# Kernel optimization log

Hardware: AMD Instinct MI355X
Metric: run time of the kernel (lower is better)

The kernel has to match this reference:

```python
import jax, jax.numpy as jnp
import numpy as np
import math

HEAD_DEPTH = 16
CLIP = 10.0
NEG_INF = 1.0e10
# combined scale: (1/sqrt(head_depth)) * log_50(400)
SCALE = (math.log(400.0) / math.log(50.0)) / math.sqrt(HEAD_DEPTH)


def setup_inputs() -> dict:
    key = jax.random.key(0)
    kq, kk, kv, km = jax.random.split(key, 4)
    B, H, S, D = 4, 8, 2048, HEAD_DEPTH
    Q = jax.random.normal(kq, (B, H, S, D), dtype=jnp.float32)
    K = jax.random.normal(kk, (B, H, S, D), dtype=jnp.float32)
    V = jax.random.normal(kv, (B, H, S, D), dtype=jnp.float32)
    # mask: (B, n_nodes, 1) bool; True -> masked (logit set to -inf)
    mask = jax.random.randint(km, (B, S, 1), 0, 2) == 1
    return {"Q": Q, "K": K, "V": V, "mask": mask}


def reference(Q, K, V, mask):
    # logits: (B, H, q_seq, k_seq)
    logits = jnp.einsum("bhqd,bhkd->bhqk", Q, K) * SCALE
    logits = CLIP * jnp.tanh(logits)  # tanh clip
    # mask[:, None, None, :, 0] -> (B, 1, 1, k_seq), True gets -inf
    m = mask[:, None, None, :, 0]
    logits = jnp.where(m, -NEG_INF, logits)
    probs = jax.nn.softmax(logits, axis=-1)
    return jnp.einsum("bhqk,bhkd->bhqd", probs, V)
```

## Files before the change

kernel.cpp:

```cpp
#include <hip/hip_runtime.h>


typedef __fp16 h2 __attribute__((ext_vector_type(2)));
typedef __fp16 h4 __attribute__((ext_vector_type(4)));
typedef float  f4 __attribute__((ext_vector_type(4)));

#define SEQ 2048
#define NBH 32
#define TPB 128
#define KWS_BYTES ((size_t)NBH * TPB * 64 * 8)
#define VWS_BYTES KWS_BYTES
#define BIAS_BYTES ((size_t)4 * SEQ * 4)
#define IDX_BYTES  ((size_t)4 * SEQ * 4)
#define META_BYTES 64
#define WS_NEEDED (KWS_BYTES + VWS_BYTES + BIAS_BYTES + IDX_BYTES + META_BYTES)

__device__ __forceinline__ float fast_exp2(float x) {
#if __has_builtin(__builtin_amdgcn_exp2f)
    return __builtin_amdgcn_exp2f(x);
#else
    return exp2f(x);
#endif
}

__device__ __forceinline__ float dot2acc(h2 a, float accv) {
#if __has_builtin(__builtin_amdgcn_fdot2)
    const h2 one = {(__fp16)1.0f, (__fp16)1.0f};
    return __builtin_amdgcn_fdot2(a, one, accv, false);
#else
    return accv + (float)a[0] + (float)a[1];
#endif
}

__global__ __launch_bounds__(256) void attn_scan(
    const int* __restrict__ maskp, int* __restrict__ idxws,
    float* __restrict__ biasws, int* __restrict__ meta)
{
    __shared__ int partial[256];
    const int b   = blockIdx.x;
    const int tid = threadIdx.x;

    int keep[8], cnt = 0;
    #pragma unroll
    for (int j = 0; j < 8; ++j) {
        keep[j] = (maskp[b * SEQ + tid * 8 + j] == 0);
        cnt += keep[j];
    }
    partial[tid] = cnt;
    __syncthreads();
    for (int off = 1; off < 256; off <<= 1) {
        int add = (tid >= off) ? partial[tid - off] : 0;
        __syncthreads();
        partial[tid] += add;
        __syncthreads();
    }
    const int total = partial[255];
    int pos = partial[tid] - cnt;
    #pragma unroll
    for (int j = 0; j < 8; ++j) {
        if (keep[j]) idxws[b * SEQ + pos++] = tid * 8 + j;
    }
    for (int i = tid; i < SEQ; i += 256) {
        biasws[b * SEQ + i] = (i < total) ? 0.0f : -1.0e30f;
        if (i >= total) idxws[b * SEQ + i] = 0;
    }
    if (tid == 0) {
        int nr = (total + 255) >> 8;
        meta[b] = nr < 1 ? 1 : nr;
    }
}

__global__ __launch_bounds__(256) void attn_prep(
    const float* __restrict__ Kp, const float* __restrict__ Vp,
    const int* __restrict__ idxws,
    __fp16* __restrict__ Kws, __fp16* __restrict__ Vws)
{
    const int tid = threadIdx.x;
    const int T   = blockIdx.x * 4 + (tid >> 6);
    const int l   = tid & 63;
    const int bh  = T >> 7;
    const int t   = T & (TPB - 1);
    const int b   = bh >> 3;
    const int c   = l & 15;
    const int g   = l >> 4;
    const size_t base = (size_t)bh * (SEQ * 16);
    const int*   idx  = idxws + (size_t)b * SEQ;

    {
        const int krow = idx[t * 16 + c];
        f4 kv = *(const f4*)(Kp + base + (size_t)krow * 16 + 4 * g);
        h2 k0 = __builtin_amdgcn_cvt_pkrtz(kv[0], kv[1]);
        h2 k1 = __builtin_amdgcn_cvt_pkrtz(kv[2], kv[3]);
        h4 kh; kh[0] = k0[0]; kh[1] = k0[1]; kh[2] = k1[0]; kh[3] = k1[1];
        *(h4*)(Kws + ((size_t)T * 64 + l) * 4) = kh;
    }
    {
        const int v0 = idx[t * 16 + 4 * g + 0];
        const int v1 = idx[t * 16 + 4 * g + 1];
        const int v2 = idx[t * 16 + 4 * g + 2];
        const int v3 = idx[t * 16 + 4 * g + 3];
        h2 p0 = __builtin_amdgcn_cvt_pkrtz(Vp[base + (size_t)v0 * 16 + c],
                                           Vp[base + (size_t)v1 * 16 + c]);
        h2 p1 = __builtin_amdgcn_cvt_pkrtz(Vp[base + (size_t)v2 * 16 + c],
                                           Vp[base + (size_t)v3 * 16 + c]);
        h4 vh; vh[0] = p0[0]; vh[1] = p0[1]; vh[2] = p1[0]; vh[3] = p1[1];
        *(h4*)(Vws + ((size_t)T * 64 + l) * 4) = vh;
    }
}

__global__ __launch_bounds__(512, 8) void attn_v5(
    const float* __restrict__ Qp, const __fp16* __restrict__ Kws,
    const __fp16* __restrict__ Vws, const float* __restrict__ biasws,
    const int* __restrict__ meta, float* __restrict__ out)
{
    __shared__ __align__(16) _Float16 Kbuf[2][4096];
    __shared__ __align__(16) _Float16 Vbuf[2][4096];
    __shared__ __align__(16) float    Bbuf[2][256];

    const int bid  = blockIdx.x;
    const int bh   = bid >> 5;
    const int qblk = bid & 31;
    const int b    = bh >> 3;
    const int tid  = threadIdx.x;
    const int wave = tid >> 6;
    const int lane = tid & 63;
    const int qt   = wave & 3;
    const int kg   = wave >> 2;
    const int c    = lane & 15;
    const int g    = lane >> 4;

    const size_t base  = (size_t)bh * (SEQ * 16);
    const int    qbase = qblk * 64 + qt * 16;
    const float  c1 = 1.1047809f;
    const float  c2 = -28.8539008f;

    const int nr = meta[b];

    h4 qfrag;
    {
        f4 qv = *(const f4*)(Qp + base + (size_t)(qbase + c) * 16 + 4 * g);
        h2 lo = __builtin_amdgcn_cvt_pkrtz(c1 * qv[0], c1 * qv[1]);
        h2 hi = __builtin_amdgcn_cvt_pkrtz(c1 * qv[2], c1 * qv[3]);
        qfrag[0] = lo[0]; qfrag[1] = lo[1]; qfrag[2] = hi[0]; qfrag[3] = hi[1];
    }

    const f4* ksrc = (const f4*)(Kws + (size_t)bh * TPB * 256);
    const f4* vsrc = (const f4*)(Vws + (size_t)bh * TPB * 256);
    const float* bsrc = biasws + (size_t)b * SEQ;

    f4 kpre = ksrc[tid];
    f4 vpre = vsrc[tid];
    float bpre = (tid < 256) ? bsrc[tid] : 0.0f;
    *(f4*)&Kbuf[0][tid * 8] = kpre;
    *(f4*)&Vbuf[0][tid * 8] = vpre;
    if (tid < 256) Bbuf[0][tid] = bpre;
    {
        const int r1 = (1 < nr) ? 1 : (nr - 1);
        kpre = ksrc[r1 * 512 + tid];
        vpre = vsrc[r1 * 512 + tid];
        if (tid < 256) bpre = bsrc[r1 * 256 + tid];
    }
    __syncthreads();

    f4 acc = {0.f, 0.f, 0.f, 0.f};
    float dsum = 0.f;

    for (int r = 0; r < nr; ++r) {
        const int cb = r & 1, nb = cb ^ 1;
        if (r + 1 < nr) {
            *(f4*)&Kbuf[nb][tid * 8] = kpre;
            *(f4*)&Vbuf[nb][tid * 8] = vpre;
            if (tid < 256) Bbuf[nb][tid] = bpre;
        }
        if (r + 2 < nr) {
            kpre = ksrc[(r + 2) * 512 + tid];
            vpre = vsrc[(r + 2) * 512 + tid];
            if (tid < 256) bpre = bsrc[(r + 2) * 256 + tid];
        }

        const _Float16* Kc = &Kbuf[cb][kg * 2048];
        const _Float16* Vc = &Vbuf[cb][kg * 2048];
        const float*    Bc = &Bbuf[cb][kg * 128];

        #pragma unroll
        for (int t = 0; t < 8; ++t) {
            h4 afrag = *(const h4*)(Kc + t * 256 + lane * 4);
            f4 s = __builtin_amdgcn_mfma_f32_16x16x16f16(
                afrag, qfrag, (f4){0.f, 0.f, 0.f, 0.f}, 0, 0, 0);

            f4 b4 = *(const f4*)(Bc + t * 16 + 4 * g);
            float p[4];
            #pragma unroll
            for (int i = 0; i < 4; ++i) {
                float tt = fast_exp2(s[i]);
                float w  = __builtin_amdgcn_rcpf(1.0f + tt);
                p[i] = fast_exp2(__builtin_fmaf(c2, w, b4[i]));
            }
            h2 plo = __builtin_amdgcn_cvt_pkrtz(p[0], p[1]);
            h2 phi = __builtin_amdgcn_cvt_pkrtz(p[2], p[3]);
            dsum = dot2acc(plo, dsum);
            dsum = dot2acc(phi, dsum);
            h4 pf; pf[0] = plo[0]; pf[1] = plo[1]; pf[2] = phi[0]; pf[3] = phi[1];

            h4 vfrag = *(const h4*)(Vc + t * 256 + lane * 4);
            acc = __builtin_amdgcn_mfma_f32_16x16x16f16(pf, vfrag, acc, 0, 0, 0);
        }
        __syncthreads();
    }

    dsum += __shfl_xor(dsum, 16);
    dsum += __shfl_xor(dsum, 32);

    float* ex = (float*)&Kbuf[0][0];
    const int slot = (qt * 64 + lane) * 5;
    if (kg == 1) {
        ex[slot + 0] = acc[0]; ex[slot + 1] = acc[1];
        ex[slot + 2] = acc[2]; ex[slot + 3] = acc[3];
        ex[slot + 4] = dsum;
    }
    __syncthreads();
    if (kg == 0) {
        const float dT = dsum + ex[slot + 4];
        #pragma unroll
        for (int i = 0; i < 4; ++i) {
            const float denom = __shfl(dT, 4 * g + i);
            out[base + (size_t)(qbase + 4 * g + i) * 16 + c] =
                (acc[i] + ex[slot + i]) / denom;
        }
    }
}

#define KROW 20
#define VROW 520

__global__ __launch_bounds__(512, 8) void attn_fwd_v3(
    const float* __restrict__ Qp, const float* __restrict__ Kp,
    const float* __restrict__ Vp, const int* __restrict__ maskp,
    float* __restrict__ out)
{
    __shared__ __align__(16) _Float16 Klds[512 * KROW];
    __shared__ __align__(16) _Float16 Vt[16 * VROW];
    __shared__ __align__(16) float biasf[512];

    const int bid  = blockIdx.x;
    const int bh   = bid >> 5;
    const int qblk = bid & 31;
    const int b    = bh >> 3;
    const int tid  = threadIdx.x;
    const int wave = tid >> 6;
    const int lane = tid & 63;
    const int qt   = wave & 3;
    const int kg   = wave >> 2;
    const int c    = lane & 15;
    const int g    = lane >> 4;

    const size_t base = (size_t)bh * (SEQ * 16);
    const int qbase = qblk * 64 + qt * 16;
    const float c1 = 1.1047809f;
    const float c2 = -28.8539008f;

    h4 qfrag;
    {
        f4 qv = *(const f4*)(Qp + base + (size_t)(qbase + c) * 16 + 4 * g);
        h2 lo = __builtin_amdgcn_cvt_pkrtz(c1 * qv[0], c1 * qv[1]);
        h2 hi = __builtin_amdgcn_cvt_pkrtz(c1 * qv[2], c1 * qv[3]);
        qfrag[0] = lo[0]; qfrag[1] = lo[1]; qfrag[2] = hi[0]; qfrag[3] = hi[1];
    }

    f4 acc = {0.f, 0.f, 0.f, 0.f};
    float dsum = 0.f;
    const int kgb = kg * 256;

    for (int round = 0; round < 4; ++round) {
        {
            const float* Kc = Kp + base + (size_t)round * (512 * 16);
            const float* Vc = Vp + base + (size_t)round * (512 * 16);
            #pragma unroll
            for (int j = 0; j < 4; ++j) {
                const int i = j * 512 + tid;
                f4 kv = *(const f4*)(Kc + (size_t)i * 4);
                f4 vv = *(const f4*)(Vc + (size_t)i * 4);
                const int key = i >> 2;
                const int dq  = (i & 3) * 4;
                h2 k0 = __builtin_amdgcn_cvt_pkrtz(kv[0], kv[1]);
                h2 k1 = __builtin_amdgcn_cvt_pkrtz(kv[2], kv[3]);
                h4 kh; kh[0] = k0[0]; kh[1] = k0[1]; kh[2] = k1[0]; kh[3] = k1[1];
                *(h4*)&Klds[key * KROW + dq] = kh;
                #pragma unroll
                for (int e = 0; e < 4; ++e)
                    Vt[(dq + e) * VROW + key] = (_Float16)vv[e];
            }
            biasf[tid] = maskp[(size_t)b * SEQ + round * 512 + tid] ? -60.0f : 0.0f;
        }
        __syncthreads();

        #pragma unroll
        for (int t = 0; t < 16; ++t) {
            const int kb = kgb + t * 16;
            h4 afrag = *(const h4*)&Klds[(kb + c) * KROW + 4 * g];
            f4 s = __builtin_amdgcn_mfma_f32_16x16x16f16(
                afrag, qfrag, (f4){0.f, 0.f, 0.f, 0.f}, 0, 0, 0);
            f4 b4 = *(const f4*)&biasf[kb + 4 * g];
            float p[4];
            #pragma unroll
            for (int i = 0; i < 4; ++i) {
                float tt = fast_exp2(s[i]);
                float w  = __builtin_amdgcn_rcpf(1.0f + tt);
                p[i] = fast_exp2(__builtin_fmaf(c2, w, b4[i]));
            }
            h2 plo = __builtin_amdgcn_cvt_pkrtz(p[0], p[1]);
            h2 phi = __builtin_amdgcn_cvt_pkrtz(p[2], p[3]);
            dsum = dot2acc(plo, dsum);
            dsum = dot2acc(phi, dsum);
            h4 pf; pf[0] = plo[0]; pf[1] = plo[1]; pf[2] = phi[0]; pf[3] = phi[1];
            h4 vfrag = *(const h4*)&Vt[c * VROW + kb + 4 * g];
            acc = __builtin_amdgcn_mfma_f32_16x16x16f16(pf, vfrag, acc, 0, 0, 0);
        }
        __syncthreads();
    }

    dsum += __shfl_xor(dsum, 16);
    dsum += __shfl_xor(dsum, 32);

    float* ex = (float*)Klds;
    const int slot = (qt * 64 + lane) * 5;
    if (kg == 1) {
        ex[slot + 0] = acc[0]; ex[slot + 1] = acc[1];
        ex[slot + 2] = acc[2]; ex[slot + 3] = acc[3];
        ex[slot + 4] = dsum;
    }
    __syncthreads();
    if (kg == 0) {
        const float dT = dsum + ex[slot + 4];
        #pragma unroll
        for (int i = 0; i < 4; ++i) {
            const float denom = __shfl(dT, 4 * g + i);
            out[base + (size_t)(qbase + 4 * g + i) * 16 + c] =
                (acc[i] + ex[slot + i]) / denom;
        }
    }
}

extern "C" void kernel_launch(void* const* d_in, const int* in_sizes, int n_in,
                              void* d_out, int out_size, void* d_ws, size_t ws_size,
                              hipStream_t stream) {
    const float* Q    = (const float*)d_in[0];
    const float* K    = (const float*)d_in[1];
    const float* V    = (const float*)d_in[2];
    const int*   mask = (const int*)d_in[3];
    float* out = (float*)d_out;

    if (ws_size >= WS_NEEDED) {
        char* p = (char*)d_ws;
        __fp16* Kws = (__fp16*)p;                       p += KWS_BYTES;
        __fp16* Vws = (__fp16*)p;                       p += VWS_BYTES;
        float*  Bws = (float*)p;                        p += BIAS_BYTES;
        int*    Iws = (int*)p;                          p += IDX_BYTES;
        int*    Mws = (int*)p;
        attn_scan<<<dim3(4), dim3(256), 0, stream>>>(mask, Iws, Bws, Mws);
        attn_prep<<<dim3(1024), dim3(256), 0, stream>>>(K, V, Iws, Kws, Vws);
        attn_v5<<<dim3(1024), dim3(512), 0, stream>>>(Q, Kws, Vws, Bws, Mws, out);
    } else {
        attn_fwd_v3<<<dim3(1024), dim3(512), 0, stream>>>(Q, K, V, mask, out);
    }
}
```

Measured before the change: 93.38 us.

## Load K/V fragments directly from global into registers, drop LDS staging

The attention kernel no longer stages K, V and bias tiles through double-buffered shared memory with per-round barriers. Each wave now reads its MFMA fragments straight from the pre-packed global workspace into a two-slot register prefetch ring, loading two tiles ahead. This removes the LDS writes and reads and the __syncthreads inside the loop. In exchange, the four query-tile waves that share a key group each fetch the same K/V data from global memory separately, so the kernel leans on L1/L2 hits and has less latency hiding.

```diff
diff --git a/kernel.cpp b/kernel.cpp
--- a/kernel.cpp
+++ b/kernel.cpp
@@ -108,14 +108,12 @@
     }
 }
 
-__global__ __launch_bounds__(512, 8) void attn_v5(
+__global__ __launch_bounds__(512, 8) void attn_v6(
     const float* __restrict__ Qp, const __fp16* __restrict__ Kws,
     const __fp16* __restrict__ Vws, const float* __restrict__ biasws,
     const int* __restrict__ meta, float* __restrict__ out)
 {
-    __shared__ __align__(16) _Float16 Kbuf[2][4096];
-    __shared__ __align__(16) _Float16 Vbuf[2][4096];
-    __shared__ __align__(16) float    Bbuf[2][256];
+    __shared__ float ex[1280];
 
     const int bid  = blockIdx.x;
     const int bh   = bid >> 5;
@@ -144,57 +142,52 @@
         qfrag[0] = lo[0]; qfrag[1] = lo[1]; qfrag[2] = hi[0]; qfrag[3] = hi[1];
     }
 
-    const f4* ksrc = (const f4*)(Kws + (size_t)bh * TPB * 256);
-    const f4* vsrc = (const f4*)(Vws + (size_t)bh * TPB * 256);
+    const h4* kf = (const h4*)(Kws + (size_t)bh * TPB * 256);
+    const h4* vf = (const h4*)(Vws + (size_t)bh * TPB * 256);
     const float* bsrc = biasws + (size_t)b * SEQ;
 
-    f4 kpre = ksrc[tid];
-    f4 vpre = vsrc[tid];
-    float bpre = (tid < 256) ? bsrc[tid] : 0.0f;
-    *(f4*)&Kbuf[0][tid * 8] = kpre;
-    *(f4*)&Vbuf[0][tid * 8] = vpre;
-    if (tid < 256) Bbuf[0][tid] = bpre;
-    {
-        const int r1 = (1 < nr) ? 1 : (nr - 1);
-        kpre = ksrc[r1 * 512 + tid];
-        vpre = vsrc[r1 * 512 + tid];
-        if (tid < 256) bpre = bsrc[r1 * 256 + tid];
-    }
-    __syncthreads();
+    const int T = nr * 8;
+    const int kgo = kg * 8;
+
+    h4 ka[2], va[2];
+    f4 ba[2];
+    {
+        const int t0 = kgo;
+        const int t1 = kgo + 1;
+        ka[0] = kf[t0 * 64 + lane]; va[0] = vf[t0 * 64 + lane];
+        ba[0] = *(const f4*)(bsrc + t0 * 16 + 4 * g);
+        ka[1] = kf[t1 * 64 + lane]; va[1] = vf[t1 * 64 + lane];
+        ba[1] = *(const f4*)(bsrc + t1 * 16 + 4 * g);
+    }
 
     f4 acc = {0.f, 0.f, 0.f, 0.f};
     float dsum = 0.f;
 
     for (int r = 0; r < nr; ++r) {
-        const int cb = r & 1, nb = cb ^ 1;
-        if (r + 1 < nr) {
-            *(f4*)&Kbuf[nb][tid * 8] = kpre;
-            *(f4*)&Vbuf[nb][tid * 8] = vpre;
-            if (tid < 256) Bbuf[nb][tid] = bpre;
-        }
-        if (r + 2 < nr) {
-            kpre = ksrc[(r + 2) * 512 + tid];
-            vpre = vsrc[(r + 2) * 512 + tid];
-            if (tid < 256) bpre = bsrc[(r + 2) * 256 + tid];
-        }
-
-        const _Float16* Kc = &Kbuf[cb][kg * 2048];
-        const _Float16* Vc = &Vbuf[cb][kg * 2048];
-        const float*    Bc = &Bbuf[cb][kg * 128];
-
         #pragma unroll
-        for (int t = 0; t < 8; ++t) {
-            h4 afrag = *(const h4*)(Kc + t * 256 + lane * 4);
+        for (int j = 0; j < 8; ++j) {
+            const int i  = r * 8 + j;
+            const int sl = i & 1;
+            const h4 afrag = ka[sl];
+            const h4 vfrag = va[sl];
+            const f4 b4    = ba[sl];
+            if (i + 2 < T) {
+                const int ip = i + 2;
+                const int tn = ((ip >> 3) << 4) + kgo + (ip & 7);
+                ka[sl] = kf[tn * 64 + lane];
+                va[sl] = vf[tn * 64 + lane];
+                ba[sl] = *(const f4*)(bsrc + tn * 16 + 4 * g);
+            }
+
             f4 s = __builtin_amdgcn_mfma_f32_16x16x16f16(
                 afrag, qfrag, (f4){0.f, 0.f, 0.f, 0.f}, 0, 0, 0);
 
-            f4 b4 = *(const f4*)(Bc + t * 16 + 4 * g);
             float p[4];
             #pragma unroll
-            for (int i = 0; i < 4; ++i) {
-                float tt = fast_exp2(s[i]);
+            for (int e = 0; e < 4; ++e) {
+                float tt = fast_exp2(s[e]);
                 float w  = __builtin_amdgcn_rcpf(1.0f + tt);
-                p[i] = fast_exp2(__builtin_fmaf(c2, w, b4[i]));
+                p[e] = fast_exp2(__builtin_fmaf(c2, w, b4[e]));
             }
             h2 plo = __builtin_amdgcn_cvt_pkrtz(p[0], p[1]);
             h2 phi = __builtin_amdgcn_cvt_pkrtz(p[2], p[3]);
@@ -202,16 +195,13 @@
             dsum = dot2acc(phi, dsum);
             h4 pf; pf[0] = plo[0]; pf[1] = plo[1]; pf[2] = phi[0]; pf[3] = phi[1];
 
-            h4 vfrag = *(const h4*)(Vc + t * 256 + lane * 4);
             acc = __builtin_amdgcn_mfma_f32_16x16x16f16(pf, vfrag, acc, 0, 0, 0);
         }
-        __syncthreads();
     }
 
     dsum += __shfl_xor(dsum, 16);
     dsum += __shfl_xor(dsum, 32);
 
-    float* ex = (float*)&Kbuf[0][0];
     const int slot = (qt * 64 + lane) * 5;
     if (kg == 1) {
         ex[slot + 0] = acc[0]; ex[slot + 1] = acc[1];
@@ -359,7 +349,7 @@
         int*    Mws = (int*)p;
         attn_scan<<<dim3(4), dim3(256), 0, stream>>>(mask, Iws, Bws, Mws);
         attn_prep<<<dim3(1024), dim3(256), 0, stream>>>(K, V, Iws, Kws, Vws);
-        attn_v5<<<dim3(1024), dim3(512), 0, stream>>>(Q, Kws, Vws, Bws, Mws, out);
+        attn_v6<<<dim3(1024), dim3(512), 0, stream>>>(Q, Kws, Vws, Bws, Mws, out);
     } else {
         attn_fwd_v3<<<dim3(1024), dim3(512), 0, stream>>>(Q, K, V, mask, out);
     }
```

After: 98.92 us. 1.06x slower.

## Use single-wave shuffle scan and skip fully masked 16-key tiles

Applied to the files above, without the earlier changes.

The mask compaction kernel becomes a single 64-lane wavefront that loads the mask with vector reads and computes the prefix sum with wave shuffles, removing the LDS and barrier-heavy block scan. It also records the number of valid 16-key tiles per batch. The attention kernel uses that count to skip MFMA and exp work on tiles past the compacted key count. Tiles are now interleaved across the two key-group waves instead of split in halves, which keeps their loads balanced. The per-tile branch adds some control overhead inside the unrolled loop.

```diff
diff --git a/kernel.cpp b/kernel.cpp
--- a/kernel.cpp
+++ b/kernel.cpp
@@ -4,6 +4,7 @@
 typedef __fp16 h2 __attribute__((ext_vector_type(2)));
 typedef __fp16 h4 __attribute__((ext_vector_type(4)));
 typedef float  f4 __attribute__((ext_vector_type(4)));
+typedef int    i4 __attribute__((ext_vector_type(4)));
 
 #define SEQ 2048
 #define NBH 32
@@ -32,41 +33,49 @@
 #endif
 }
 
-__global__ __launch_bounds__(256) void attn_scan(
+__global__ __launch_bounds__(64) void attn_scan(
     const int* __restrict__ maskp, int* __restrict__ idxws,
     float* __restrict__ biasws, int* __restrict__ meta)
 {
-    __shared__ int partial[256];
-    const int b   = blockIdx.x;
-    const int tid = threadIdx.x;
-
-    int keep[8], cnt = 0;
+    const int b = blockIdx.x;
+    const int t = threadIdx.x;
+    const i4* m4 = (const i4*)(maskp + (size_t)b * SEQ);
+
+    i4 ch[8];
+    int cnt = 0;
     #pragma unroll
     for (int j = 0; j < 8; ++j) {
-        keep[j] = (maskp[b * SEQ + tid * 8 + j] == 0);
-        cnt += keep[j];
-    }
-    partial[tid] = cnt;
-    __syncthreads();
-    for (int off = 1; off < 256; off <<= 1) {
-        int add = (tid >= off) ? partial[tid - off] : 0;
-        __syncthreads();
-        partial[tid] += add;
-        __syncthreads();
-    }
-    const int total = partial[255];
-    int pos = partial[tid] - cnt;
+        ch[j] = m4[j * 64 + t];
+        #pragma unroll
+        for (int e = 0; e < 4; ++e) cnt += (ch[j][e] == 0);
+    }
+    int incl = cnt;
+    #pragma unroll
+    for (int off = 1; off < 64; off <<= 1) {
+        int src = __shfl_up(incl, off);
+        if (t >= off) incl += src;
+    }
+    const int total = __shfl(incl, 63);
+    int pos = incl - cnt;
     #pragma unroll
     for (int j = 0; j < 8; ++j) {
-        if (keep[j]) idxws[b * SEQ + pos++] = tid * 8 + j;
-    }
-    for (int i = tid; i < SEQ; i += 256) {
-        biasws[b * SEQ + i] = (i < total) ? 0.0f : -1.0e30f;
-        if (i >= total) idxws[b * SEQ + i] = 0;
-    }
-    if (tid == 0) {
-        int nr = (total + 255) >> 8;
-        meta[b] = nr < 1 ? 1 : nr;
+        #pragma unroll
+        for (int e = 0; e < 4; ++e) {
+            if (ch[j][e] == 0)
+                idxws[(size_t)b * SEQ + pos++] = (j * 64 + t) * 4 + e;
+        }
+    }
+    #pragma unroll
+    for (int j = 0; j < 32; ++j) {
+        const int i = j * 64 + t;
+        biasws[(size_t)b * SEQ + i] = (i < total) ? 0.0f : -1.0e30f;
+        if (i >= total) idxws[(size_t)b * SEQ + i] = 0;
+    }
+    if (t == 0) {
+        int nt = (total + 15) >> 4;  if (nt < 1) nt = 1;
+        int nr = (nt + 15) >> 4;     if (nr < 1) nr = 1;
+        meta[b] = nr;
+        meta[4 + b] = nt;
     }
 }
 
@@ -108,7 +117,7 @@
     }
 }
 
-__global__ __launch_bounds__(512, 8) void attn_v5(
+__global__ __launch_bounds__(512, 8) void attn_v7(
     const float* __restrict__ Qp, const __fp16* __restrict__ Kws,
     const __fp16* __restrict__ Vws, const float* __restrict__ biasws,
     const int* __restrict__ meta, float* __restrict__ out)
@@ -135,6 +144,7 @@
     const float  c2 = -28.8539008f;
 
     const int nr = meta[b];
+    const int nt = meta[4 + b];
 
     h4 qfrag;
     {
@@ -178,32 +188,36 @@
             if (tid < 256) bpre = bsrc[(r + 2) * 256 + tid];
         }
 
-        const _Float16* Kc = &Kbuf[cb][kg * 2048];
-        const _Float16* Vc = &Vbuf[cb][kg * 2048];
-        const float*    Bc = &Bbuf[cb][kg * 128];
-
-        #pragma unroll
-        for (int t = 0; t < 8; ++t) {
-            h4 afrag = *(const h4*)(Kc + t * 256 + lane * 4);
-            f4 s = __builtin_amdgcn_mfma_f32_16x16x16f16(
-                afrag, qfrag, (f4){0.f, 0.f, 0.f, 0.f}, 0, 0, 0);
-
-            f4 b4 = *(const f4*)(Bc + t * 16 + 4 * g);
-            float p[4];
-            #pragma unroll
-            for (int i = 0; i < 4; ++i) {
-                float tt = fast_exp2(s[i]);
-                float w  = __builtin_amdgcn_rcpf(1.0f + tt);
-                p[i] = fast_exp2(__builtin_fmaf(c2, w, b4[i]));
+        const _Float16* Kc = &Kbuf[cb][0];
+        const _Float16* Vc = &Vbuf[cb][0];
+        const float*    Bc = &Bbuf[cb][0];
+        const int rbase = r << 4;
+
+        #pragma unroll
+        for (int j = 0; j < 8; ++j) {
+            const int tir = 2 * j + kg;
+            if (rbase + tir < nt) {
+                h4 afrag = *(const h4*)(Kc + tir * 256 + lane * 4);
+                f4 s = __builtin_amdgcn_mfma_f32_16x16x16f16(
+                    afrag, qfrag, (f4){0.f, 0.f, 0.f, 0.f}, 0, 0, 0);
+
+                f4 b4 = *(const f4*)(Bc + tir * 16 + 4 * g);
+                float p[4];
+                #pragma unroll
+                for (int e = 0; e < 4; ++e) {
+                    float tt = fast_exp2(s[e]);
+                    float w  = __builtin_amdgcn_rcpf(1.0f + tt);
+                    p[e] = fast_exp2(__builtin_fmaf(c2, w, b4[e]));
+                }
+                h2 plo = __builtin_amdgcn_cvt_pkrtz(p[0], p[1]);
+                h2 phi = __builtin_amdgcn_cvt_pkrtz(p[2], p[3]);
+                dsum = dot2acc(plo, dsum);
+                dsum = dot2acc(phi, dsum);
+                h4 pf; pf[0] = plo[0]; pf[1] = plo[1]; pf[2] = phi[0]; pf[3] = phi[1];
+
+                h4 vfrag = *(const h4*)(Vc + tir * 256 + lane * 4);
+                acc = __builtin_amdgcn_mfma_f32_16x16x16f16(pf, vfrag, acc, 0, 0, 0);
             }
-            h2 plo = __builtin_amdgcn_cvt_pkrtz(p[0], p[1]);
-            h2 phi = __builtin_amdgcn_cvt_pkrtz(p[2], p[3]);
-            dsum = dot2acc(plo, dsum);
-            dsum = dot2acc(phi, dsum);
-            h4 pf; pf[0] = plo[0]; pf[1] = plo[1]; pf[2] = phi[0]; pf[3] = phi[1];
-
-            h4 vfrag = *(const h4*)(Vc + t * 256 + lane * 4);
-            acc = __builtin_amdgcn_mfma_f32_16x16x16f16(pf, vfrag, acc, 0, 0, 0);
         }
         __syncthreads();
     }
@@ -357,9 +371,9 @@
         float*  Bws = (float*)p;                        p += BIAS_BYTES;
         int*    Iws = (int*)p;                          p += IDX_BYTES;
         int*    Mws = (int*)p;
-        attn_scan<<<dim3(4), dim3(256), 0, stream>>>(mask, Iws, Bws, Mws);
+        attn_scan<<<dim3(4), dim3(64), 0, stream>>>(mask, Iws, Bws, Mws);
         attn_prep<<<dim3(1024), dim3(256), 0, stream>>>(K, V, Iws, Kws, Vws);
-        attn_v5<<<dim3(1024), dim3(512), 0, stream>>>(Q, Kws, Vws, Bws, Mws, out);
+        attn_v7<<<dim3(1024), dim3(512), 0, stream>>>(Q, Kws, Vws, Bws, Mws, out);
     } else {
         attn_fwd_v3<<<dim3(1024), dim3(512), 0, stream>>>(Q, K, V, mask, out);
     }
```

Result: slower. 96.79 us (+3.7%).
